# Performance work log

Hardware: AMD Instinct MI355X
Metric: run time of the kernel (lower is better)

The kernel has to match this reference:

```python
import jax, jax.numpy as jnp
import numpy as np

B, C, H, W = 512, 1, 64, 64
T, L, Z = 32, 1024, 128
RS, WS = 12, 12


def _filterbank(g_x, g_y, logvar, logdelta, N):
    # g_x, g_y, logvar, logdelta: (B, 1)
    g_x = 0.5 * (W + 1) * (g_x + 1)
    g_y = 0.5 * (H + 1) * (g_y + 1)
    delta = (max(H, W) - 1) / (N - 1) * jnp.exp(logdelta)            # (B,1)
    offs = jnp.arange(1.0, 1.0 + N) - 0.5 * (N + 1)                  # (N,)
    mu_x = g_x + offs * delta                                        # (B,N)
    mu_y = g_y + offs * delta                                        # (B,N)
    inv2var = 0.5 / jnp.exp(logvar)[:, :, None]                      # (B,1,1)
    Fx = jnp.exp(-inv2var * (jnp.arange(1.0, 1.0 + W)[None, None, :] - mu_x[:, :, None]) ** 2)
    Fx = Fx / jnp.sum(Fx + 1e-8, axis=2, keepdims=True)              # (B,N,W)
    Fy = jnp.exp(-inv2var * (jnp.arange(1.0, 1.0 + H)[None, None, :] - mu_y[:, :, None]) ** 2)
    Fy = Fy / jnp.sum(Fy + 1e-8, axis=2, keepdims=True)              # (B,N,H)
    return Fx, Fy


def _lstm(x, h, c, Wih, Whh, bih, bhh):
    g = x @ Wih.T + bih + h @ Whh.T + bhh
    i, f, gg, o = jnp.split(g, 4, axis=1)
    c = jax.nn.sigmoid(f) * c + jax.nn.sigmoid(i) * jnp.tanh(gg)
    h = jax.nn.sigmoid(o) * jnp.tanh(c)
    return h, c


def setup_inputs() -> dict:
    key = jax.random.key(0)
    ks = jax.random.split(key, 9)
    s = 0.02
    return {
        'x': jax.random.uniform(ks[0], (B, C * H * W), jnp.float32),
        'enc_Wih': jax.random.normal(ks[1], (4 * L, 2 * RS * RS + L), jnp.float32) * s,
        'enc_Whh': jax.random.normal(ks[2], (4 * L, L), jnp.float32) * s,
        'enc_bih': jnp.zeros((4 * L,), jnp.float32),
        'enc_bhh': jnp.zeros((4 * L,), jnp.float32),
        'dec_Wih': jax.random.normal(ks[3], (4 * L, Z), jnp.float32) * s,
        'dec_Whh': jax.random.normal(ks[4], (4 * L, L), jnp.float32) * s,
        'dec_bih': jnp.zeros((4 * L,), jnp.float32),
        'dec_bhh': jnp.zeros((4 * L,), jnp.float32),
        'zW': jax.random.normal(ks[5], (2 * Z, L), jnp.float32) * s,
        'zb': jnp.zeros((2 * Z,), jnp.float32),
        'wW': jax.random.normal(ks[6], (WS * WS, L), jnp.float32) * s,
        'wb': jnp.zeros((WS * WS,), jnp.float32),
        'raW': jax.random.normal(ks[7], (5, L), jnp.float32) * s,
        'rab': jnp.zeros((5,), jnp.float32),
        'waW': jax.random.normal(ks[8], (5, L), jnp.float32) * s,
        'wab': jnp.zeros((5,), jnp.float32),
    }


def reference(x, enc_Wih, enc_Whh, enc_bih, enc_bhh, dec_Wih, dec_Whh, dec_bih, dec_bhh,
              zW, zb, wW, wb, raW, rab, waW, wab):
    def read(xf, x_hat, h_dec):
        a = h_dec @ raW.T + rab                                      # (B,5)
        g_x, g_y, logvar, logdelta, loggamma = jnp.split(a, 5, axis=1)
        Fx, Fy = _filterbank(g_x, g_y, logvar, logdelta, RS)
        nx = jnp.einsum('bnh,bhw,bmw->bnm', Fy, xf.reshape(-1, H, W), Fx)
        nxh = jnp.einsum('bnh,bhw,bmw->bnm', Fy, x_hat.reshape(-1, H, W), Fx)
        return jnp.exp(loggamma) * jnp.concatenate(
            [nx.reshape(nx.shape[0], -1), nxh.reshape(nxh.shape[0], -1)], axis=1)

    def write(h_dec):
        w = h_dec @ wW.T + wb                                        # (B, WS*WS)
        a = h_dec @ waW.T + wab
        g_x, g_y, logvar, logdelta, loggamma = jnp.split(a, 5, axis=1)
        Fx, Fy = _filterbank(g_x, g_y, logvar, logdelta, WS)
        wr = jnp.einsum('bnh,bnm,bmw->bhw', Fy, w.reshape(-1, WS, WS), Fx)
        return jnp.exp(-loggamma) * wr.reshape(wr.shape[0], -1)

    zkeys = jax.random.split(jax.random.key(42), T)

    def step(carry, key):
        c, h_enc, c_enc, h_dec, c_dec = carry
        x_hat = x - jax.nn.sigmoid(c)
        r = read(x, x_hat, h_dec)
        h_enc, c_enc = _lstm(jnp.concatenate([r, h_dec], axis=1), h_enc, c_enc,
                             enc_Wih, enc_Whh, enc_bih, enc_bhh)
        stats = h_enc @ zW.T + zb
        mu, logsig = jnp.split(stats, 2, axis=1)
        sig = jnp.exp(logsig)
        z = mu + sig * jax.random.normal(key, mu.shape, mu.dtype)
        h_dec, c_dec = _lstm(z, h_dec, c_dec, dec_Wih, dec_Whh, dec_bih, dec_bhh)
        c = c + write(h_dec)
        return (c, h_enc, c_enc, h_dec, c_dec), (mu, sig)

    c0 = jnp.zeros_like(x)
    h0 = jnp.zeros((x.shape[0], L), x.dtype)
    carry0 = (c0, h0, h0, h0, h0)
    (c, _, _, _, _), (mus, sigs) = jax.lax.scan(step, carry0, zkeys)
    # stack along last dim like torch.stack(mus, dim=-1): (B, Z, T)
    return c, jnp.moveaxis(mus, 0, -1), jnp.moveaxis(sigs, 0, -1)
```

## Files before the change

### kernel.cpp

```cpp
#include <hip/hip_runtime.h>
#include <cstdint>
#include <cstddef>

#define BB 512
#define TT 32
#define LL 1024
#define ZZ 128

typedef unsigned short ushort_t;
typedef __attribute__((ext_vector_type(8))) short s8v;
typedef __attribute__((ext_vector_type(4))) float f32x4;

__device__ __forceinline__ float sigf(float x) { return 1.0f / (1.0f + expf(-x)); }

__device__ __forceinline__ ushort_t f2bf(float f) {
  uint32_t u = __float_as_uint(f);
  uint32_t r = (u + 0x7FFFu + ((u >> 16) & 1u)) >> 16;
  return (ushort_t)r;
}
__device__ __forceinline__ float bf2f(ushort_t h) {
  return __uint_as_float(((uint32_t)h) << 16);
}
__device__ __forceinline__ void splitf(float v, ushort_t& hi, ushort_t& lo) {
  hi = f2bf(v);
  lo = f2bf(v - bf2f(hi));
}

__device__ __forceinline__ float jax_erfinv(float x) {
  float w = -log1pf(-x * x);
  float p;
  if (w < 5.0f) {
    w = w - 2.5f;
    p = 2.81022636e-08f;
    p = fmaf(p, w, 3.43273939e-07f);
    p = fmaf(p, w, -3.5233877e-06f);
    p = fmaf(p, w, -4.39150654e-06f);
    p = fmaf(p, w, 0.00021858087f);
    p = fmaf(p, w, -0.00125372503f);
    p = fmaf(p, w, -0.00417768164f);
    p = fmaf(p, w, 0.246640727f);
    p = fmaf(p, w, 1.50140941f);
  } else {
    w = sqrtf(w) - 3.0f;
    p = -0.000200214257f;
    p = fmaf(p, w, 0.000100950558f);
    p = fmaf(p, w, 0.00134934322f);
    p = fmaf(p, w, -0.00367342844f);
    p = fmaf(p, w, 0.00573950773f);
    p = fmaf(p, w, -0.0076224613f);
    p = fmaf(p, w, 0.00943887047f);
    p = fmaf(p, w, 1.00167406f);
    p = fmaf(p, w, 2.83297682f);
  }
  return p * x;
}

__device__ __forceinline__ void threefry(uint32_t k0, uint32_t k1,
                                         uint32_t x0, uint32_t x1,
                                         uint32_t& o0, uint32_t& o1) {
  uint32_t ks0 = k0, ks1 = k1, ks2 = k0 ^ k1 ^ 0x1BD11BDAu;
  x0 += ks0; x1 += ks1;
#define TF_ROT(x, d) (((x) << (d)) | ((x) >> (32 - (d))))
#define TF_RND(r) { x0 += x1; x1 = TF_ROT(x1, r); x1 ^= x0; }
  TF_RND(13) TF_RND(15) TF_RND(26) TF_RND(6)
  x0 += ks1; x1 += ks2 + 1u;
  TF_RND(17) TF_RND(29) TF_RND(16) TF_RND(24)
  x0 += ks2; x1 += ks0 + 2u;
  TF_RND(13) TF_RND(15) TF_RND(26) TF_RND(6)
  x0 += ks0; x1 += ks1 + 3u;
  TF_RND(17) TF_RND(29) TF_RND(16) TF_RND(24)
  x0 += ks1; x1 += ks2 + 4u;
  TF_RND(13) TF_RND(15) TF_RND(26) TF_RND(6)
  x0 += ks2; x1 += ks0 + 5u;
#undef TF_RND
#undef TF_ROT
  o0 = x0; o1 = x1;
}

__device__ __forceinline__ float bits_to_normal(uint32_t bits) {
  uint32_t fb = (bits >> 9) | 0x3f800000u;
  float f = __uint_as_float(fb) - 1.0f;
  const float lo = -0.99999994f;
  float u = fmaxf(lo, f * 2.0f + lo);
  return 1.41421356237f * jax_erfinv(u);
}

__global__ __launch_bounds__(256) void k_split(const float* __restrict__ src,
                                               ushort_t* __restrict__ hi,
                                               ushort_t* __restrict__ lo, int n) {
  int i = blockIdx.x * 256 + threadIdx.x;
  if (i >= n) return;
  ushort_t h, l;
  splitf(src[i], h, l);
  hi[i] = h; lo[i] = l;
}

__global__ void k_catbias(const float* __restrict__ wb, const float* __restrict__ wab,
                          float* __restrict__ cb) {
  int i = threadIdx.x;
  cb[i] = (i < 144) ? wb[i] : (i < 149 ? wab[i - 144] : 0.f);
}

struct Seg { const ushort_t* A; const ushort_t* W; int K; int lda; int ldw; };
struct SegList { Seg s[9]; int n; };

__device__ __forceinline__ void load_tiles(const Seg& sg, int bm, int bn, int N, int k0,
                                           int tid, s8v va[4], s8v vw[4]) {
#pragma unroll
  for (int i = 0; i < 4; ++i) {
    int cch = tid + 256 * i;
    int row = cch >> 3, col = cch & 7;
    va[i] = *(const s8v*)(sg.A + (size_t)(bm + row) * sg.lda + k0 + col * 8);
    int n = bn + row;
    if (n < N) vw[i] = *(const s8v*)(sg.W + (size_t)n * sg.ldw + k0 + col * 8);
    else       vw[i] = (s8v)(short)0;
  }
}

__global__ __launch_bounds__(256, 2) void mfma_gemm(
    float* __restrict__ C, unsigned zstride, int N, SegList segs, int ipz, int T) {
  __shared__ __align__(16) ushort_t As[128][72];
  __shared__ __align__(16) ushort_t Ws[128][72];
  const int z = blockIdx.z;
  C += (size_t)z * zstride;
  const int bm = blockIdx.y * 128, bn = blockIdx.x * 128;
  const int tid = threadIdx.x;
  const int w = tid >> 6, lane = tid & 63;
  const int wr = w >> 1, wc = w & 1;
  const int lr = lane & 15, lq = lane >> 4;
  f32x4 acc[4][4] = {};

  int it0 = z * ipz;
  int it1 = it0 + ipz; if (it1 > T) it1 = T;
  int iters = it1 - it0;
  if (iters > 0) {
    int si = 0, rem = it0;
    while (rem >= (segs.s[si].K >> 6)) { rem -= segs.s[si].K >> 6; ++si; }
    int k0 = rem << 6;
    s8v va[4], vw[4];
    load_tiles(segs.s[si], bm, bn, N, k0, tid, va, vw);
    for (int it = 0; it < iters; ++it) {
      __syncthreads();
#pragma unroll
      for (int i = 0; i < 4; ++i) {
        int cch = tid + 256 * i;
        *(s8v*)&As[cch >> 3][(cch & 7) * 8] = va[i];
        *(s8v*)&Ws[cch >> 3][(cch & 7) * 8] = vw[i];
      }
      __syncthreads();
      int nsi = si, nk0 = k0 + 64;
      if (nk0 >= segs.s[si].K) { nk0 = 0; ++nsi; }
      if (it + 1 < iters) load_tiles(segs.s[nsi], bm, bn, N, nk0, tid, va, vw);
#pragma unroll
      for (int ks = 0; ks < 2; ++ks) {
        s8v af[4], bf[4];
#pragma unroll
        for (int m = 0; m < 4; ++m)
          af[m] = *(const s8v*)&As[wr * 64 + m * 16 + lr][ks * 32 + lq * 8];
#pragma unroll
        for (int j = 0; j < 4; ++j)
          bf[j] = *(const s8v*)&Ws[wc * 64 + j * 16 + lr][ks * 32 + lq * 8];
#pragma unroll
        for (int m = 0; m < 4; ++m)
#pragma unroll
          for (int j = 0; j < 4; ++j)
            acc[m][j] = __builtin_amdgcn_mfma_f32_16x16x32_bf16(af[m], bf[j], acc[m][j], 0, 0, 0);
      }
      si = nsi; k0 = nk0;
    }
  }
#pragma unroll
  for (int j = 0; j < 4; ++j) {
    int col = bn + wc * 64 + j * 16 + lr;
    if (col < N) {
#pragma unroll
      for (int m = 0; m < 4; ++m)
#pragma unroll
        for (int q = 0; q < 4; ++q) {
          int rr = bm + wr * 64 + m * 16 + lq * 4 + q;
          C[(size_t)rr * N + col] = acc[m][j][q];
        }
    }
  }
}

__global__ __launch_bounds__(256) void k_fread(
    const float* __restrict__ x, const float* __restrict__ c,
    const float* __restrict__ ra5, const float* __restrict__ rab,
    ushort_t* __restrict__ rH, ushort_t* __restrict__ rL) {
  int b = blockIdx.x;
  __shared__ float a_sh[5];
  __shared__ float fx[12][64], fy[12][64];
  __shared__ float srow[24];
  __shared__ float X[64][64];
  __shared__ float Xh[64][64];
  __shared__ float tmp[12][64], tmph[12][64];
  int tid = threadIdx.x;
  if (tid < 5) a_sh[tid] = ra5[b * 8 + tid] + rab[tid];
  for (int e = tid; e < 4096; e += 256) {
    float xv = x[(size_t)b * 4096 + e];
    float cv = c[(size_t)b * 4096 + e];
    X[e >> 6][e & 63] = xv;
    Xh[e >> 6][e & 63] = xv - sigf(cv);
  }
  __syncthreads();
  float gx = 32.5f * (a_sh[0] + 1.f);
  float gy = 32.5f * (a_sh[1] + 1.f);
  float i2v = 0.5f * expf(-a_sh[2]);
  float delta = (63.f / 11.f) * expf(a_sh[3]);
  float gam = expf(a_sh[4]);
  for (int e = tid; e < 768; e += 256) {
    int n = e >> 6, p = e & 63;
    float mu_x = gx + ((float)n - 5.5f) * delta;
    float mu_y = gy + ((float)n - 5.5f) * delta;
    float dx = (float)(p + 1) - mu_x;
    float dy = (float)(p + 1) - mu_y;
    fx[n][p] = expf(-i2v * dx * dx);
    fy[n][p] = expf(-i2v * dy * dy);
  }
  __syncthreads();
  if (tid < 24) {
    int n = tid % 12;
    float s = 0.f;
    if (tid < 12) { for (int p = 0; p < 64; ++p) s += fx[n][p]; }
    else          { for (int p = 0; p < 64; ++p) s += fy[n][p]; }
    srow[tid] = s + 6.4e-7f;
  }
  __syncthreads();
  for (int e = tid; e < 768; e += 256) {
    int n = e >> 6, p = e & 63;
    fx[n][p] /= srow[n];
    fy[n][p] /= srow[12 + n];
  }
  __syncthreads();
  for (int e = tid; e < 768; e += 256) {
    int n = e >> 6, w2 = e & 63;
    float s = 0.f, sh = 0.f;
    for (int hh = 0; hh < 64; ++hh) {
      float f = fy[n][hh];
      s  = fmaf(f, X[hh][w2], s);
      sh = fmaf(f, Xh[hh][w2], sh);
    }
    tmp[n][w2] = s; tmph[n][w2] = sh;
  }
  __syncthreads();
  if (tid < 144) {
    int n = tid / 12, m = tid % 12;
    float s = 0.f, sh = 0.f;
    for (int w2 = 0; w2 < 64; ++w2) {
      float f = fx[m][w2];
      s  = fmaf(tmp[n][w2], f, s);
      sh = fmaf(tmph[n][w2], f, sh);
    }
    float v0 = gam * s, v1 = gam * sh;
    size_t i0 = (size_t)b * 320 + n * 12 + m;
    size_t i1 = i0 + 144;
    ushort_t h0, l0, h1, l1;
    splitf(v0, h0, l0); splitf(v1, h1, l1);
    rH[i0] = h0; rL[i0] = l0;
    rH[i1] = h1; rL[i1] = l1;
  }
}

__global__ __launch_bounds__(256) void k_z(const float* __restrict__ parts,
                                           unsigned SZ, int nz,
                                           const float* __restrict__ zb,
                                           ushort_t* __restrict__ zH,
                                           ushort_t* __restrict__ zL,
                                           float* __restrict__ out_mu,
                                           float* __restrict__ out_sg, int t) {
  int i = blockIdx.x * 256 + threadIdx.x;
  int b = i >> 7, zi = i & 127;
  float mu = zb[zi], ls = zb[128 + zi];
  for (int z = 0; z < nz; ++z) {
    size_t base = (size_t)z * SZ + (size_t)b * 256;
    mu += parts[base + zi];
    ls += parts[base + 128 + zi];
  }
  uint32_t kA, kB, o0, o1;
  threefry(0u, 42u, 0u, (uint32_t)t, kA, kB);
  threefry(kA, kB, 0u, (uint32_t)i, o0, o1);
  float ep = bits_to_normal(o0 ^ o1);
  float sg = expf(ls);
  float zv = mu + sg * ep;
  ushort_t zh, zl;
  splitf(zv, zh, zl);
  zH[i] = zh; zL[i] = zl;
  out_mu[(size_t)b * 4096 + zi * 32 + t] = mu;
  out_sg[(size_t)b * 4096 + zi * 32 + t] = sg;
}

__global__ __launch_bounds__(256) void k_fwrite(
    float* __restrict__ c, const float* __restrict__ parts, unsigned WZ, int nz,
    const float* __restrict__ cb, float* __restrict__ ra5) {
  int b = blockIdx.x;
  __shared__ float red[160];
  __shared__ float fx[12][64], fy[12][64];
  __shared__ float srow[24];
  __shared__ float tmp[12][64];
  int tid = threadIdx.x;
  if (tid < 154) {
    float s = cb[tid];
    for (int z = 0; z < nz; ++z) s += parts[(size_t)z * WZ + (size_t)b * 176 + tid];
    red[tid] = s;
    if (tid >= 149) ra5[b * 8 + tid - 149] = s;
  }
  __syncthreads();
  float gx = 32.5f * (red[144] + 1.f);
  float gy = 32.5f * (red[145] + 1.f);
  float i2v = 0.5f * expf(-red[146]);
  float delta = (63.f / 11.f) * expf(red[147]);
  float gam = expf(-red[148]);
  for (int e = tid; e < 768; e += 256) {
    int n = e >> 6, p = e & 63;
    float mu_x = gx + ((float)n - 5.5f) * delta;
    float mu_y = gy + ((float)n - 5.5f) * delta;
    float dx = (float)(p + 1) - mu_x;
    float dy = (float)(p + 1) - mu_y;
    fx[n][p] = expf(-i2v * dx * dx);
    fy[n][p] = expf(-i2v * dy * dy);
  }
  __syncthreads();
  if (tid < 24) {
    int n = tid % 12;
    float s = 0.f;
    if (tid < 12) { for (int p = 0; p < 64; ++p) s += fx[n][p]; }
    else          { for (int p = 0; p < 64; ++p) s += fy[n][p]; }
    srow[tid] = s + 6.4e-7f;
  }
  __syncthreads();
  for (int e = tid; e < 768; e += 256) {
    int n = e >> 6, p = e & 63;
    fx[n][p] /= srow[n];
    fy[n][p] /= srow[12 + n];
  }
  __syncthreads();
  for (int e = tid; e < 768; e += 256) {
    int n = e >> 6, w2 = e & 63;
    float s = 0.f;
#pragma unroll
    for (int m = 0; m < 12; ++m) s = fmaf(red[n * 12 + m], fx[m][w2], s);
    tmp[n][w2] = s;
  }
  __syncthreads();
  for (int e = tid; e < 4096; e += 256) {
    int hh = e >> 6, w2 = e & 63;
    float s = 0.f;
#pragma unroll
    for (int n = 0; n < 12; ++n) s = fmaf(fy[n][hh], tmp[n][w2], s);
    c[(size_t)b * 4096 + e] += gam * s;
  }
}

__global__ __launch_bounds__(256) void k_lstm(const float* __restrict__ g,
                                              unsigned GZ, int nz,
                                              const float* __restrict__ bih,
                                              const float* __restrict__ bhh,
                                              float* __restrict__ cst,
                                              ushort_t* __restrict__ hH,
                                              ushort_t* __restrict__ hL) {
  int i = blockIdx.x * 256 + threadIdx.x;
  int b = i >> 10, u = i & 1023;
  size_t base = (size_t)b * 4096;
  float ig = bih[u]        + bhh[u];
  float fg = bih[1024 + u] + bhh[1024 + u];
  float gg = bih[2048 + u] + bhh[2048 + u];
  float og = bih[3072 + u] + bhh[3072 + u];
  for (int z = 0; z < nz; ++z) {
    const float* gz = g + (size_t)z * GZ + base;
    ig += gz[u]; fg += gz[1024 + u]; gg += gz[2048 + u]; og += gz[3072 + u];
  }
  float cv = sigf(fg) * cst[i] + sigf(ig) * tanhf(gg);
  cst[i] = cv;
  float hv = sigf(og) * tanhf(cv);
  ushort_t hh, hl;
  splitf(hv, hh, hl);
  hH[i] = hh; hL[i] = hl;
}

extern "C" void kernel_launch(void* const* d_in, const int* in_sizes, int n_in,
                              void* d_out, int out_size, void* d_ws, size_t ws_size,
                              hipStream_t stream) {
  const float* x       = (const float*)d_in[0];
  const float* enc_Wih = (const float*)d_in[1];
  const float* enc_Whh = (const float*)d_in[2];
  const float* enc_bih = (const float*)d_in[3];
  const float* enc_bhh = (const float*)d_in[4];
  const float* dec_Wih = (const float*)d_in[5];
  const float* dec_Whh = (const float*)d_in[6];
  const float* dec_bih = (const float*)d_in[7];
  const float* dec_bhh = (const float*)d_in[8];
  const float* zW  = (const float*)d_in[9];
  const float* zb  = (const float*)d_in[10];
  const float* wW  = (const float*)d_in[11];
  const float* wb  = (const float*)d_in[12];
  const float* raW = (const float*)d_in[13];
  const float* rab = (const float*)d_in[14];
  const float* waW = (const float*)d_in[15];
  const float* wab = (const float*)d_in[16];

  float* out = (float*)d_out;
  float* c      = out;
  float* out_mu = out + 2097152;
  float* out_sg = out + 4194304;

  int NZ = 4;
  size_t need = 0;
  for (int pass = 0; pass < 2; ++pass) {
    size_t off = 0;
    auto sz = [&](size_t bytes) { off = (off + bytes + 255) & ~(size_t)255; };
    sz(2097152); sz(2097152);
    sz(1048576); sz(1048576); sz(1048576); sz(1048576);
    sz(327680); sz(327680);
    sz(360448); sz(360448);
    sz(16384);
    sz(131072); sz(131072);
    sz((size_t)NZ * 8388608);
    sz(704);
    sz(10747904); sz(10747904);
    sz(8388608); sz(8388608);
    sz(1048576); sz(1048576);
    sz(8388608); sz(8388608);
    sz(524288); sz(524288);
    need = off;
    if (pass == 0 && ws_size < need) NZ = 2; else break;
  }

  char* base = (char*)d_ws;
  size_t off = 0;
  auto alloc = [&](size_t bytes) -> char* {
    char* p = base + off;
    off = (off + bytes + 255) & ~(size_t)255;
    return p;
  };
  float* c_enc = (float*)alloc(2097152);
  float* c_dec = (float*)alloc(2097152);
  ushort_t* hdH = (ushort_t*)alloc(1048576);
  ushort_t* hdL = (ushort_t*)alloc(1048576);
  ushort_t* heH = (ushort_t*)alloc(1048576);
  ushort_t* heL = (ushort_t*)alloc(1048576);
  ushort_t* rH  = (ushort_t*)alloc(327680);
  ushort_t* rL  = (ushort_t*)alloc(327680);
  ushort_t* cWH = (ushort_t*)alloc(360448);
  ushort_t* cWL = (ushort_t*)alloc(360448);
  float* ra5    = (float*)alloc(16384);
  size_t zero_bytes = off;
  ushort_t* zH = (ushort_t*)alloc(131072);
  ushort_t* zL = (ushort_t*)alloc(131072);
  float* gbuf  = (float*)alloc((size_t)NZ * 8388608);
  float* cb    = (float*)alloc(704);
  ushort_t* eWihH = (ushort_t*)alloc(10747904);
  ushort_t* eWihL = (ushort_t*)alloc(10747904);
  ushort_t* eWhhH = (ushort_t*)alloc(8388608);
  ushort_t* eWhhL = (ushort_t*)alloc(8388608);
  ushort_t* dWihH = (ushort_t*)alloc(1048576);
  ushort_t* dWihL = (ushort_t*)alloc(1048576);
  ushort_t* dWhhH = (ushort_t*)alloc(8388608);
  ushort_t* dWhhL = (ushort_t*)alloc(8388608);
  ushort_t* zWH   = (ushort_t*)alloc(524288);
  ushort_t* zWL   = (ushort_t*)alloc(524288);

  hipMemsetAsync(c, 0, (size_t)2097152 * sizeof(float), stream);
  hipMemsetAsync(base, 0, zero_bytes, stream);

  k_split<<<(5373952 + 255) / 256, 256, 0, stream>>>(enc_Wih, eWihH, eWihL, 5373952);
  k_split<<<(4194304 + 255) / 256, 256, 0, stream>>>(enc_Whh, eWhhH, eWhhL, 4194304);
  k_split<<<(524288 + 255) / 256, 256, 0, stream>>>(dec_Wih, dWihH, dWihL, 524288);
  k_split<<<(4194304 + 255) / 256, 256, 0, stream>>>(dec_Whh, dWhhH, dWhhL, 4194304);
  k_split<<<(262144 + 255) / 256, 256, 0, stream>>>(zW, zWH, zWL, 262144);
  k_split<<<(147456 + 255) / 256, 256, 0, stream>>>(wW, cWH, cWL, 147456);
  k_split<<<(5120 + 255) / 256, 256, 0, stream>>>(waW, cWH + 147456, cWL + 147456, 5120);
  k_split<<<(5120 + 255) / 256, 256, 0, stream>>>(raW, cWH + 152576, cWL + 152576, 5120);
  k_catbias<<<1, 176, 0, stream>>>(wb, wab, cb);

  SegList encS;
  encS.n = 9;
  encS.s[0] = {rH,  eWihH,       320,  320, 1312};
  encS.s[1] = {rL,  eWihH,       320,  320, 1312};
  encS.s[2] = {rH,  eWihL,       320,  320, 1312};
  encS.s[3] = {hdH, eWihH + 288, 1024, 1024, 1312};
  encS.s[4] = {hdL, eWihH + 288, 1024, 1024, 1312};
  encS.s[5] = {hdH, eWihL + 288, 1024, 1024, 1312};
  encS.s[6] = {heH, eWhhH,       1024, 1024, 1024};
  encS.s[7] = {heL, eWhhH,       1024, 1024, 1024};
  encS.s[8] = {heH, eWhhL,       1024, 1024, 1024};
  SegList decS;
  decS.n = 6;
  decS.s[0] = {zH,  dWihH, 128,  128, 128};
  decS.s[1] = {zL,  dWihH, 128,  128, 128};
  decS.s[2] = {zH,  dWihL, 128,  128, 128};
  decS.s[3] = {hdH, dWhhH, 1024, 1024, 1024};
  decS.s[4] = {hdL, dWhhH, 1024, 1024, 1024};
  decS.s[5] = {hdH, dWhhL, 1024, 1024, 1024};
  SegList staS;
  staS.n = 3;
  staS.s[0] = {heH, zWH, 1024, 1024, 1024};
  staS.s[1] = {heL, zWH, 1024, 1024, 1024};
  staS.s[2] = {heH, zWL, 1024, 1024, 1024};
  SegList wvS;
  wvS.n = 3;
  wvS.s[0] = {hdH, cWH, 1024, 1024, 1024};
  wvS.s[1] = {hdL, cWH, 1024, 1024, 1024};
  wvS.s[2] = {hdH, cWL, 1024, 1024, 1024};

  const unsigned GZ = 2097152;
  const unsigned SZ = 131072;
  const unsigned WZ = 90112;
  const int ipz_e = (111 + NZ - 1) / NZ;
  const int ipz_d = (54 + NZ - 1) / NZ;

  for (int t = 0; t < TT; ++t) {
    k_fread<<<512, 256, 0, stream>>>(x, c, ra5, rab, rH, rL);
    mfma_gemm<<<dim3(32, 4, NZ), 256, 0, stream>>>(gbuf, GZ, 4096, encS, ipz_e, 111);
    k_lstm<<<2048, 256, 0, stream>>>(gbuf, GZ, NZ, enc_bih, enc_bhh, c_enc, heH, heL);
    mfma_gemm<<<dim3(2, 4, 8), 256, 0, stream>>>(gbuf, SZ, 256, staS, 6, 48);
    k_z<<<256, 256, 0, stream>>>(gbuf, SZ, 8, zb, zH, zL, out_mu, out_sg, t);
    mfma_gemm<<<dim3(32, 4, NZ), 256, 0, stream>>>(gbuf, GZ, 4096, decS, ipz_d, 54);
    k_lstm<<<2048, 256, 0, stream>>>(gbuf, GZ, NZ, dec_bih, dec_bhh, c_dec, hdH, hdL);
    mfma_gemm<<<dim3(2, 4, 8), 256, 0, stream>>>(gbuf, WZ, 176, wvS, 6, 48);
    k_fwrite<<<512, 256, 0, stream>>>(c, gbuf, WZ, 8, cb, ra5);
  }
}
```

Before: 4.047 ms.

## Fuse next-step read into write kernel and vectorize LSTM cell kernel

The glimpse read for step t+1 is merged into the write kernel of step t, so the updated canvas stays in shared memory and is not re-read from global memory. This removes one launch per step and the ra5 round trip through the workspace. The first read before the loop now runs with the initial attention parameters, which come from the bias alone. The LSTM cell kernel also processes four units per thread with float4 loads and stores, but the larger shared footprint of the fused kernel may lower occupancy.

```diff
diff --git a/kernel.cpp b/kernel.cpp
--- a/kernel.cpp
+++ b/kernel.cpp
@@ -186,7 +186,7 @@
 
 __global__ __launch_bounds__(256) void k_fread(
     const float* __restrict__ x, const float* __restrict__ c,
-    const float* __restrict__ ra5, const float* __restrict__ rab,
+    const float* __restrict__ rab,
     ushort_t* __restrict__ rH, ushort_t* __restrict__ rL) {
   int b = blockIdx.x;
   __shared__ float a_sh[5];
@@ -196,7 +196,7 @@
   __shared__ float Xh[64][64];
   __shared__ float tmp[12][64], tmph[12][64];
   int tid = threadIdx.x;
-  if (tid < 5) a_sh[tid] = ra5[b * 8 + tid] + rab[tid];
+  if (tid < 5) a_sh[tid] = rab[tid];
   for (int e = tid; e < 4096; e += 256) {
     float xv = x[(size_t)b * 4096 + e];
     float cv = c[(size_t)b * 4096 + e];
@@ -290,35 +290,40 @@
   out_sg[(size_t)b * 4096 + zi * 32 + t] = sg;
 }
 
-__global__ __launch_bounds__(256) void k_fwrite(
-    float* __restrict__ c, const float* __restrict__ parts, unsigned WZ, int nz,
-    const float* __restrict__ cb, float* __restrict__ ra5) {
+__global__ __launch_bounds__(256) void k_fwr(
+    float* __restrict__ c, const float* __restrict__ x,
+    const float* __restrict__ parts, unsigned WZ, int nz,
+    const float* __restrict__ cb, const float* __restrict__ rab,
+    ushort_t* __restrict__ rH, ushort_t* __restrict__ rL, int last) {
   int b = blockIdx.x;
   __shared__ float red[160];
+  __shared__ float a_sh[5];
   __shared__ float fx[12][64], fy[12][64];
   __shared__ float srow[24];
-  __shared__ float tmp[12][64];
+  __shared__ float tmp[12][64], tmph[12][64];
+  __shared__ float X[64][64];
+  __shared__ float Xh[64][64];
   int tid = threadIdx.x;
   if (tid < 154) {
     float s = cb[tid];
     for (int z = 0; z < nz; ++z) s += parts[(size_t)z * WZ + (size_t)b * 176 + tid];
     red[tid] = s;
-    if (tid >= 149) ra5[b * 8 + tid - 149] = s;
-  }
-  __syncthreads();
-  float gx = 32.5f * (red[144] + 1.f);
-  float gy = 32.5f * (red[145] + 1.f);
-  float i2v = 0.5f * expf(-red[146]);
-  float delta = (63.f / 11.f) * expf(red[147]);
-  float gam = expf(-red[148]);
-  for (int e = tid; e < 768; e += 256) {
-    int n = e >> 6, p = e & 63;
-    float mu_x = gx + ((float)n - 5.5f) * delta;
-    float mu_y = gy + ((float)n - 5.5f) * delta;
-    float dx = (float)(p + 1) - mu_x;
-    float dy = (float)(p + 1) - mu_y;
-    fx[n][p] = expf(-i2v * dx * dx);
-    fy[n][p] = expf(-i2v * dy * dy);
+  }
+  __syncthreads();
+  {
+    float gx = 32.5f * (red[144] + 1.f);
+    float gy = 32.5f * (red[145] + 1.f);
+    float i2v = 0.5f * expf(-red[146]);
+    float delta = (63.f / 11.f) * expf(red[147]);
+    for (int e = tid; e < 768; e += 256) {
+      int n = e >> 6, p = e & 63;
+      float mu_x = gx + ((float)n - 5.5f) * delta;
+      float mu_y = gy + ((float)n - 5.5f) * delta;
+      float dx = (float)(p + 1) - mu_x;
+      float dy = (float)(p + 1) - mu_y;
+      fx[n][p] = expf(-i2v * dx * dx);
+      fy[n][p] = expf(-i2v * dy * dy);
+    }
   }
   __syncthreads();
   if (tid < 24) {
@@ -343,15 +348,84 @@
     tmp[n][w2] = s;
   }
   __syncthreads();
-  for (int e = tid; e < 4096; e += 256) {
-    int hh = e >> 6, w2 = e & 63;
+  {
+    float gam = expf(-red[148]);
+    for (int e = tid; e < 4096; e += 256) {
+      int hh = e >> 6, w2 = e & 63;
+      float s = 0.f;
+#pragma unroll
+      for (int n = 0; n < 12; ++n) s = fmaf(fy[n][hh], tmp[n][w2], s);
+      float cv = c[(size_t)b * 4096 + e] + gam * s;
+      c[(size_t)b * 4096 + e] = cv;
+      float xv = x[(size_t)b * 4096 + e];
+      X[hh][w2] = xv;
+      Xh[hh][w2] = xv - sigf(cv);
+    }
+  }
+  if (last) return;
+  if (tid < 5) a_sh[tid] = red[149 + tid] + rab[tid];
+  __syncthreads();
+  {
+    float gx = 32.5f * (a_sh[0] + 1.f);
+    float gy = 32.5f * (a_sh[1] + 1.f);
+    float i2v = 0.5f * expf(-a_sh[2]);
+    float delta = (63.f / 11.f) * expf(a_sh[3]);
+    for (int e = tid; e < 768; e += 256) {
+      int n = e >> 6, p = e & 63;
+      float mu_x = gx + ((float)n - 5.5f) * delta;
+      float mu_y = gy + ((float)n - 5.5f) * delta;
+      float dx = (float)(p + 1) - mu_x;
+      float dy = (float)(p + 1) - mu_y;
+      fx[n][p] = expf(-i2v * dx * dx);
+      fy[n][p] = expf(-i2v * dy * dy);
+    }
+  }
+  __syncthreads();
+  if (tid < 24) {
+    int n = tid % 12;
     float s = 0.f;
-#pragma unroll
-    for (int n = 0; n < 12; ++n) s = fmaf(fy[n][hh], tmp[n][w2], s);
-    c[(size_t)b * 4096 + e] += gam * s;
-  }
-}
-
+    if (tid < 12) { for (int p = 0; p < 64; ++p) s += fx[n][p]; }
+    else          { for (int p = 0; p < 64; ++p) s += fy[n][p]; }
+    srow[tid] = s + 6.4e-7f;
+  }
+  __syncthreads();
+  for (int e = tid; e < 768; e += 256) {
+    int n = e >> 6, p = e & 63;
+    fx[n][p] /= srow[n];
+    fy[n][p] /= srow[12 + n];
+  }
+  __syncthreads();
+  for (int e = tid; e < 768; e += 256) {
+    int n = e >> 6, w2 = e & 63;
+    float s = 0.f, sh = 0.f;
+    for (int hh = 0; hh < 64; ++hh) {
+      float f = fy[n][hh];
+      s  = fmaf(f, X[hh][w2], s);
+      sh = fmaf(f, Xh[hh][w2], sh);
+    }
+    tmp[n][w2] = s; tmph[n][w2] = sh;
+  }
+  __syncthreads();
+  if (tid < 144) {
+    float gam = expf(a_sh[4]);
+    int n = tid / 12, m = tid % 12;
+    float s = 0.f, sh = 0.f;
+    for (int w2 = 0; w2 < 64; ++w2) {
+      float f = fx[m][w2];
+      s  = fmaf(tmp[n][w2], f, s);
+      sh = fmaf(tmph[n][w2], f, sh);
+    }
+    float v0 = gam * s, v1 = gam * sh;
+    size_t i0 = (size_t)b * 320 + n * 12 + m;
+    size_t i1 = i0 + 144;
+    ushort_t h0, l0, h1, l1;
+    splitf(v0, h0, l0); splitf(v1, h1, l1);
+    rH[i0] = h0; rL[i0] = l0;
+    rH[i1] = h1; rL[i1] = l1;
+  }
+}
+
+typedef unsigned short us4 __attribute__((ext_vector_type(4)));
 __global__ __launch_bounds__(256) void k_lstm(const float* __restrict__ g,
                                               unsigned GZ, int nz,
                                               const float* __restrict__ bih,
@@ -359,23 +433,54 @@
                                               float* __restrict__ cst,
                                               ushort_t* __restrict__ hH,
                                               ushort_t* __restrict__ hL) {
-  int i = blockIdx.x * 256 + threadIdx.x;
-  int b = i >> 10, u = i & 1023;
-  size_t base = (size_t)b * 4096;
-  float ig = bih[u]        + bhh[u];
-  float fg = bih[1024 + u] + bhh[1024 + u];
-  float gg = bih[2048 + u] + bhh[2048 + u];
-  float og = bih[3072 + u] + bhh[3072 + u];
+  int q = blockIdx.x * 256 + threadIdx.x;
+  int b = q >> 8, uq = q & 255;
+  size_t base = (size_t)b * 1024;
+  float4 ig = *(const float4*)&bih[uq * 4];
+  float4 fg = *(const float4*)&bih[1024 + uq * 4];
+  float4 gg = *(const float4*)&bih[2048 + uq * 4];
+  float4 og = *(const float4*)&bih[3072 + uq * 4];
+  {
+    float4 t0 = *(const float4*)&bhh[uq * 4];
+    float4 t1 = *(const float4*)&bhh[1024 + uq * 4];
+    float4 t2 = *(const float4*)&bhh[2048 + uq * 4];
+    float4 t3 = *(const float4*)&bhh[3072 + uq * 4];
+    ig.x += t0.x; ig.y += t0.y; ig.z += t0.z; ig.w += t0.w;
+    fg.x += t1.x; fg.y += t1.y; fg.z += t1.z; fg.w += t1.w;
+    gg.x += t2.x; gg.y += t2.y; gg.z += t2.z; gg.w += t2.w;
+    og.x += t3.x; og.y += t3.y; og.z += t3.z; og.w += t3.w;
+  }
   for (int z = 0; z < nz; ++z) {
-    const float* gz = g + (size_t)z * GZ + base;
-    ig += gz[u]; fg += gz[1024 + u]; gg += gz[2048 + u]; og += gz[3072 + u];
-  }
-  float cv = sigf(fg) * cst[i] + sigf(ig) * tanhf(gg);
-  cst[i] = cv;
-  float hv = sigf(og) * tanhf(cv);
-  ushort_t hh, hl;
-  splitf(hv, hh, hl);
-  hH[i] = hh; hL[i] = hl;
+    const float* gz = g + (size_t)z * GZ + base * 4;
+    float4 t0 = *(const float4*)&gz[uq * 4];
+    float4 t1 = *(const float4*)&gz[1024 + uq * 4];
+    float4 t2 = *(const float4*)&gz[2048 + uq * 4];
+    float4 t3 = *(const float4*)&gz[3072 + uq * 4];
+    ig.x += t0.x; ig.y += t0.y; ig.z += t0.z; ig.w += t0.w;
+    fg.x += t1.x; fg.y += t1.y; fg.z += t1.z; fg.w += t1.w;
+    gg.x += t2.x; gg.y += t2.y; gg.z += t2.z; gg.w += t2.w;
+    og.x += t3.x; og.y += t3.y; og.z += t3.z; og.w += t3.w;
+  }
+  float4 cv = *(const float4*)&cst[(size_t)q * 4];
+  float cva[4] = {cv.x, cv.y, cv.z, cv.w};
+  float iga[4] = {ig.x, ig.y, ig.z, ig.w};
+  float fga[4] = {fg.x, fg.y, fg.z, fg.w};
+  float gga[4] = {gg.x, gg.y, gg.z, gg.w};
+  float oga[4] = {og.x, og.y, og.z, og.w};
+  us4 hhv, hlv;
+  float cvo[4];
+#pragma unroll
+  for (int j = 0; j < 4; ++j) {
+    float cnew = sigf(fga[j]) * cva[j] + sigf(iga[j]) * tanhf(gga[j]);
+    cvo[j] = cnew;
+    float hv = sigf(oga[j]) * tanhf(cnew);
+    ushort_t hh, hl;
+    splitf(hv, hh, hl);
+    hhv[j] = hh; hlv[j] = hl;
+  }
+  *(float4*)&cst[(size_t)q * 4] = make_float4(cvo[0], cvo[1], cvo[2], cvo[3]);
+  *(us4*)&hH[(size_t)q * 4] = hhv;
+  *(us4*)&hL[(size_t)q * 4] = hlv;
 }
 
 extern "C" void kernel_launch(void* const* d_in, const int* in_sizes, int n_in,
@@ -413,7 +518,6 @@
     sz(1048576); sz(1048576); sz(1048576); sz(1048576);
     sz(327680); sz(327680);
     sz(360448); sz(360448);
-    sz(16384);
     sz(131072); sz(131072);
     sz((size_t)NZ * 8388608);
     sz(704);
@@ -443,7 +547,6 @@
   ushort_t* rL  = (ushort_t*)alloc(327680);
   ushort_t* cWH = (ushort_t*)alloc(360448);
   ushort_t* cWL = (ushort_t*)alloc(360448);
-  float* ra5    = (float*)alloc(16384);
   size_t zero_bytes = off;
   ushort_t* zH = (ushort_t*)alloc(131072);
   ushort_t* zL = (ushort_t*)alloc(131072);
@@ -509,15 +612,15 @@
   const int ipz_e = (111 + NZ - 1) / NZ;
   const int ipz_d = (54 + NZ - 1) / NZ;
 
+  k_fread<<<512, 256, 0, stream>>>(x, c, rab, rH, rL);
   for (int t = 0; t < TT; ++t) {
-    k_fread<<<512, 256, 0, stream>>>(x, c, ra5, rab, rH, rL);
     mfma_gemm<<<dim3(32, 4, NZ), 256, 0, stream>>>(gbuf, GZ, 4096, encS, ipz_e, 111);
-    k_lstm<<<2048, 256, 0, stream>>>(gbuf, GZ, NZ, enc_bih, enc_bhh, c_enc, heH, heL);
+    k_lstm<<<512, 256, 0, stream>>>(gbuf, GZ, NZ, enc_bih, enc_bhh, c_enc, heH, heL);
     mfma_gemm<<<dim3(2, 4, 8), 256, 0, stream>>>(gbuf, SZ, 256, staS, 6, 48);
     k_z<<<256, 256, 0, stream>>>(gbuf, SZ, 8, zb, zH, zL, out_mu, out_sg, t);
     mfma_gemm<<<dim3(32, 4, NZ), 256, 0, stream>>>(gbuf, GZ, 4096, decS, ipz_d, 54);
-    k_lstm<<<2048, 256, 0, stream>>>(gbuf, GZ, NZ, dec_bih, dec_bhh, c_dec, hdH, hdL);
+    k_lstm<<<512, 256, 0, stream>>>(gbuf, GZ, NZ, dec_bih, dec_bhh, c_dec, hdH, hdL);
     mfma_gemm<<<dim3(2, 4, 8), 256, 0, stream>>>(gbuf, WZ, 176, wvS, 6, 48);
-    k_fwrite<<<512, 256, 0, stream>>>(c, gbuf, WZ, 8, cb, ra5);
-  }
-}
+    k_fwr<<<512, 256, 0, stream>>>(c, x, gbuf, WZ, 8, cb, rab, rH, rL, t == TT - 1);
+  }
+}
```

New measurement: 3.918 ms. -3.2%, faster.
